# Performance work log

Hardware: AMD Instinct MI355X
Metric: run time of the kernel (lower is better)

Reference implementation:

```python
import jax, jax.numpy as jnp
import numpy as np

N_NODES = 50000
N_EDGES = 1600000
IN_SIZE = 128
NUM_HEADS = 4
OUT_SIZE = 32


def setup_inputs() -> dict:
    key = jax.random.key(0)
    k1, k2, k3, k4 = jax.random.split(key, 4)
    feat = jax.random.normal(k1, (N_NODES, IN_SIZE), dtype=jnp.float32)
    src = jax.random.randint(k2, (N_EDGES,), 0, N_NODES)
    dst = jnp.sort(jax.random.randint(k3, (N_EDGES,), 0, N_NODES))
    # fc weight of DGL DotGatConv: Linear(in_size, num_heads*out_size, bias=False)
    W = jax.random.normal(k4, (IN_SIZE, NUM_HEADS * OUT_SIZE), dtype=jnp.float32) * 0.05
    return {"feat": feat, "src": src, "dst": dst, "W": W}


def reference(feat, src, dst, W):
    N = feat.shape[0]
    H, D = NUM_HEADS, OUT_SIZE
    # project: [N, H, D]
    h = (feat @ W).reshape(N, H, D)
    h_src = h[src]            # [E, H, D] gather
    h_dst = h[dst]            # [E, H, D] gather
    # per-edge dot-product attention score, scaled by sqrt(out_size)
    e = jnp.sum(h_src * h_dst, axis=-1) / jnp.sqrt(jnp.asarray(D, h.dtype))  # [E, H]
    # edge softmax over incoming edges of each destination node
    m = jax.ops.segment_max(e, dst, num_segments=N)        # [N, H]
    ex = jnp.exp(e - m[dst])                               # [E, H]
    s = jax.ops.segment_sum(ex, dst, num_segments=N)       # [N, H]
    alpha = ex / s[dst]                                    # [E, H]
    # weighted aggregation of source features: sum_e alpha_e * h_src_e -> dst
    out = jax.ops.segment_sum(alpha[:, :, None] * h_src, dst, num_segments=N)  # [N, H, D]
    return out
```

## Files before the change

### kernel.cpp

```cpp
#include <hip/hip_runtime.h>
#include <math.h>

#define N_NODES 50000
#define N_EDGES 1600000
#define IN_SIZE 128
#define HD 128
#define NUM_HEADS 4
#define OUT_SIZE 32
#define STRIPS (N_NODES / 16)
#define STRIPS_PER_WAVE 3

#define SCALE2 0.25503486f

typedef __attribute__((ext_vector_type(8))) short short8;
typedef __attribute__((ext_vector_type(4))) float floatx4;

static __device__ __forceinline__ unsigned bf16rne(float f) {
    unsigned u = __float_as_uint(f);
    u += 0x7FFF + ((u >> 16) & 1);
    return u >> 16;
}
static __device__ __forceinline__ float bf16lo(unsigned u) {
    return __uint_as_float(u << 16);
}
static __device__ __forceinline__ float bf16hi(unsigned u) {
    return __uint_as_float(u & 0xFFFF0000u);
}

__global__ __launch_bounds__(256) void k_init(const float* __restrict__ W,
                                              const int* __restrict__ dst,
                                              unsigned short* __restrict__ WT,
                                              int* __restrict__ off) {
    int i = blockIdx.x * 256 + threadIdx.x;
    if (i < IN_SIZE * HD) {
        int c = i >> 7, k = i & 127;
        WT[c * IN_SIZE + k] = (unsigned short)bf16rne(W[k * HD + c]);
    }
    if (i <= N_NODES) {
        int lo = 0, hi = N_EDGES;
        while (lo < hi) {
            int mid = (lo + hi) >> 1;
            if (dst[mid] < i) lo = mid + 1; else hi = mid;
        }
        off[i] = lo;
    }
}

__global__ __launch_bounds__(256, 1) void k_proj(const float* __restrict__ feat,
                                                 const unsigned short* __restrict__ WT,
                                                 unsigned short* __restrict__ hb) {
    int wid = (blockIdx.x * 256 + threadIdx.x) >> 6;
    int lane = threadIdx.x & 63;
    int s0 = wid * STRIPS_PER_WAVE;
    if (s0 >= STRIPS) return;
    int quad = lane >> 4;
    int l15 = lane & 15;

    short8 Bf[8][4];
#pragma unroll
    for (int t = 0; t < 8; t++) {
#pragma unroll
        for (int kb = 0; kb < 4; kb++) {
            union { uint4 v; short8 s; } u;
            u.v = *(const uint4*)(WT + (size_t)(t * 16 + l15) * IN_SIZE + kb * 32 + quad * 8);
            Bf[t][kb] = u.s;
        }
    }

    for (int it = 0; it < STRIPS_PER_WAVE; it++) {
        int strip = s0 + it;
        if (strip >= STRIPS) break;
        int row = strip * 16 + l15;

        const float* ab = feat + (size_t)row * IN_SIZE + quad * 8;
        float4 a[8];
#pragma unroll
        for (int kb = 0; kb < 4; kb++) {
            a[2 * kb]     = *(const float4*)(ab + kb * 32);
            a[2 * kb + 1] = *(const float4*)(ab + kb * 32 + 4);
        }

        floatx4 acc[8];
#pragma unroll
        for (int t = 0; t < 8; t++) acc[t] = (floatx4)(0.f);

#pragma unroll
        for (int kb = 0; kb < 4; kb++) {
            float4 x = a[2 * kb], y = a[2 * kb + 1];
            union { short8 s; unsigned u[4]; } af;
            af.u[0] = bf16rne(x.x) | (bf16rne(x.y) << 16);
            af.u[1] = bf16rne(x.z) | (bf16rne(x.w) << 16);
            af.u[2] = bf16rne(y.x) | (bf16rne(y.y) << 16);
            af.u[3] = bf16rne(y.z) | (bf16rne(y.w) << 16);
#pragma unroll
            for (int t = 0; t < 8; t++)
                acc[t] = __builtin_amdgcn_mfma_f32_16x16x32_bf16(af.s, Bf[t][kb], acc[t], 0, 0, 0);
        }

#pragma unroll
        for (int t = 0; t < 8; t++) {
#pragma unroll
            for (int r = 0; r < 4; r++) {
                int R = strip * 16 + quad * 4 + r;
                hb[(size_t)R * HD + t * 16 + l15] = (unsigned short)bf16rne(acc[t][r]);
            }
        }
    }
}

__global__ __launch_bounds__(256) void k_edge(const unsigned short* __restrict__ hb,
                                              const int* __restrict__ src,
                                              const int* __restrict__ off,
                                              float* __restrict__ out) {
    int n = (blockIdx.x * 256 + threadIdx.x) >> 6;
    int lane = threadIdx.x & 63;
    if (n >= N_NODES) return;
    int e0 = off[n], e1 = off[n + 1];

    int g = lane >> 4;
    int p = lane & 15;

    const uint4* h4 = (const uint4*)hb;
    uint4 hdv = h4[(size_t)n * 16 + p];
    float hd[8];
#pragma unroll
    for (int d = 0; d < 4; d++) {
        unsigned u = ((const unsigned*)&hdv)[d];
        hd[2 * d]     = bf16lo(u) * SCALE2;
        hd[2 * d + 1] = bf16hi(u) * SCALE2;
    }

    float s = 0.f;
    float acc[8];
#pragma unroll
    for (int i = 0; i < 8; i++) acc[i] = 0.f;

    int iters = (e1 - e0 + 3) >> 2;
    int e = e0 + g;
    bool act = (e < e1);
    int si = act ? src[e] : n;
    uint4 a = h4[(size_t)si * 16 + p];

    for (int it = 0; it < iters; it++) {
        int en = e + 4;
        bool act_n = (en < e1);
        int si_n = act_n ? src[en] : n;
        uint4 b = h4[(size_t)si_n * 16 + p];

        float av[8];
#pragma unroll
        for (int d = 0; d < 4; d++) {
            unsigned u = ((const unsigned*)&a)[d];
            av[2 * d]     = bf16lo(u);
            av[2 * d + 1] = bf16hi(u);
        }
        float pd = 0.f;
#pragma unroll
        for (int i = 0; i < 8; i++) pd = fmaf(av[i], hd[i], pd);
        pd += __shfl_xor(pd, 1);
        pd += __shfl_xor(pd, 2);

        float sc = fminf(pd, 30.f);
        float w = act ? __builtin_amdgcn_exp2f(sc) : 0.f;
        s += w;
#pragma unroll
        for (int i = 0; i < 8; i++) acc[i] = fmaf(w, av[i], acc[i]);

        a = b; act = act_n; e = en;
    }

#pragma unroll
    for (int d = 16; d <= 32; d <<= 1) {
        s += __shfl_xor(s, d);
#pragma unroll
        for (int i = 0; i < 8; i++) acc[i] += __shfl_xor(acc[i], d);
    }

    if (g == 0) {
        float inv = (s > 0.f) ? 1.f / s : 0.f;
        float4 o0, o1;
        o0.x = acc[0] * inv; o0.y = acc[1] * inv; o0.z = acc[2] * inv; o0.w = acc[3] * inv;
        o1.x = acc[4] * inv; o1.y = acc[5] * inv; o1.z = acc[6] * inv; o1.w = acc[7] * inv;
        float4* op = (float4*)(out + (size_t)n * HD + 8 * p);
        op[0] = o0;
        op[1] = o1;
    }
}

extern "C" void kernel_launch(void* const* d_in, const int* in_sizes, int n_in,
                              void* d_out, int out_size, void* d_ws, size_t ws_size,
                              hipStream_t stream) {
    const float* feat = (const float*)d_in[0];
    const int*   src  = (const int*)d_in[1];
    const int*   dst  = (const int*)d_in[2];
    const float* W    = (const float*)d_in[3];
    float* out = (float*)d_out;

    char* ws = (char*)d_ws;
    unsigned short* hb = (unsigned short*)ws;
    unsigned short* WT = (unsigned short*)(ws + (size_t)N_NODES * HD * 2);
    int* off = (int*)(ws + (size_t)N_NODES * HD * 2 + IN_SIZE * HD * 2);

    k_init<<<(N_NODES + 1 + 255) / 256, 256, 0, stream>>>(W, dst, WT, off);
    int proj_waves = (STRIPS + STRIPS_PER_WAVE - 1) / STRIPS_PER_WAVE;
    k_proj<<<(proj_waves + 3) / 4, 256, 0, stream>>>(feat, WT, hb);
    k_edge<<<(N_NODES + 3) / 4, 256, 0, stream>>>(hb, src, off, out);
}
```

Measured before the change: 154.7 us.

## Split projected features per head and assign one wave per (head, node)

New measurement: 189.8 us. 1.23x slower.

```diff
diff --git a/kernel.cpp b/kernel.cpp
--- a/kernel.cpp
+++ b/kernel.cpp
@@ -9,6 +9,9 @@
 #define OUT_SIZE 32
 #define STRIPS (N_NODES / 16)
 #define STRIPS_PER_WAVE 3
+#define PROJ_WAVES ((STRIPS + STRIPS_PER_WAVE - 1) / STRIPS_PER_WAVE)
+#define PROJ_BLOCKS ((PROJ_WAVES + 3) / 4)
+#define OFF_BLOCKS ((N_NODES + 1 + 255) / 256)
 
 #define SCALE2 0.25503486f
 
@@ -27,29 +30,25 @@
     return __uint_as_float(u & 0xFFFF0000u);
 }
 
-__global__ __launch_bounds__(256) void k_init(const float* __restrict__ W,
-                                              const int* __restrict__ dst,
-                                              unsigned short* __restrict__ WT,
-                                              int* __restrict__ off) {
-    int i = blockIdx.x * 256 + threadIdx.x;
-    if (i < IN_SIZE * HD) {
-        int c = i >> 7, k = i & 127;
-        WT[c * IN_SIZE + k] = (unsigned short)bf16rne(W[k * HD + c]);
-    }
-    if (i <= N_NODES) {
-        int lo = 0, hi = N_EDGES;
-        while (lo < hi) {
-            int mid = (lo + hi) >> 1;
-            if (dst[mid] < i) lo = mid + 1; else hi = mid;
-        }
-        off[i] = lo;
-    }
-}
-
-__global__ __launch_bounds__(256, 1) void k_proj(const float* __restrict__ feat,
-                                                 const unsigned short* __restrict__ WT,
-                                                 unsigned short* __restrict__ hb) {
-    int wid = (blockIdx.x * 256 + threadIdx.x) >> 6;
+__global__ __launch_bounds__(256, 1) void k_pre(const float* __restrict__ feat,
+                                                const float* __restrict__ W,
+                                                const int* __restrict__ dst,
+                                                unsigned short* __restrict__ hh,
+                                                int* __restrict__ off) {
+    if (blockIdx.x >= PROJ_BLOCKS) {
+        int i = (blockIdx.x - PROJ_BLOCKS) * 256 + threadIdx.x;
+        if (i <= N_NODES) {
+            int lo = 0, hi = N_EDGES;
+            while (lo < hi) {
+                int mid = (lo + hi) >> 1;
+                if (dst[mid] < i) lo = mid + 1; else hi = mid;
+            }
+            off[i] = lo;
+        }
+        return;
+    }
+
+    int wid = blockIdx.x * 4 + (threadIdx.x >> 6);
     int lane = threadIdx.x & 63;
     int s0 = wid * STRIPS_PER_WAVE;
     if (s0 >= STRIPS) return;
@@ -61,9 +60,15 @@
     for (int t = 0; t < 8; t++) {
 #pragma unroll
         for (int kb = 0; kb < 4; kb++) {
-            union { uint4 v; short8 s; } u;
-            u.v = *(const uint4*)(WT + (size_t)(t * 16 + l15) * IN_SIZE + kb * 32 + quad * 8);
-            Bf[t][kb] = u.s;
+            union { short8 s; unsigned u[4]; } bu;
+#pragma unroll
+            for (int jj = 0; jj < 4; jj++) {
+                int k0 = kb * 32 + quad * 8 + 2 * jj;
+                float lo = W[(size_t)k0 * HD + t * 16 + l15];
+                float hi = W[(size_t)(k0 + 1) * HD + t * 16 + l15];
+                bu.u[jj] = bf16rne(lo) | (bf16rne(hi) << 16);
+            }
+            Bf[t][kb] = bu.s;
         }
     }
 
@@ -102,32 +107,37 @@
 #pragma unroll
             for (int r = 0; r < 4; r++) {
                 int R = strip * 16 + quad * 4 + r;
-                hb[(size_t)R * HD + t * 16 + l15] = (unsigned short)bf16rne(acc[t][r]);
+                hh[((size_t)(t >> 1) * N_NODES + R) * 32 + (t & 1) * 16 + l15] =
+                    (unsigned short)bf16rne(acc[t][r]);
             }
         }
     }
 }
 
-__global__ __launch_bounds__(256) void k_edge(const unsigned short* __restrict__ hb,
+__global__ __launch_bounds__(256) void k_edge(const unsigned short* __restrict__ hh,
                                               const int* __restrict__ src,
                                               const int* __restrict__ off,
                                               float* __restrict__ out) {
-    int n = (blockIdx.x * 256 + threadIdx.x) >> 6;
+    int wid = blockIdx.x * 4 + (threadIdx.x >> 6);
     int lane = threadIdx.x & 63;
-    if (n >= N_NODES) return;
+    if (wid >= 4 * N_NODES) return;
+    int hd = (wid >= 3 * N_NODES) ? 3 : (wid >= 2 * N_NODES) ? 2 : (wid >= N_NODES) ? 1 : 0;
+    int n = wid - hd * N_NODES;
+
     int e0 = off[n], e1 = off[n + 1];
-
-    int g = lane >> 4;
-    int p = lane & 15;
-
-    const uint4* h4 = (const uint4*)hb;
-    uint4 hdv = h4[(size_t)n * 16 + p];
-    float hd[8];
+    int g = lane >> 2;
+    int q = lane & 3;
+
+    const uint4* h4 = (const uint4*)hh;
+    size_t hbase = (size_t)hd * N_NODES;
+
+    uint4 hdv = h4[(hbase + n) * 4 + q];
+    float hdc[8];
 #pragma unroll
     for (int d = 0; d < 4; d++) {
         unsigned u = ((const unsigned*)&hdv)[d];
-        hd[2 * d]     = bf16lo(u) * SCALE2;
-        hd[2 * d + 1] = bf16hi(u) * SCALE2;
+        hdc[2 * d]     = bf16lo(u) * SCALE2;
+        hdc[2 * d + 1] = bf16hi(u) * SCALE2;
     }
 
     float s = 0.f;
@@ -135,17 +145,17 @@
 #pragma unroll
     for (int i = 0; i < 8; i++) acc[i] = 0.f;
 
-    int iters = (e1 - e0 + 3) >> 2;
+    int iters = (e1 - e0 + 15) >> 4;
     int e = e0 + g;
     bool act = (e < e1);
     int si = act ? src[e] : n;
-    uint4 a = h4[(size_t)si * 16 + p];
+    uint4 a = h4[(hbase + si) * 4 + q];
 
     for (int it = 0; it < iters; it++) {
-        int en = e + 4;
+        int en = e + 16;
         bool act_n = (en < e1);
         int si_n = act_n ? src[en] : n;
-        uint4 b = h4[(size_t)si_n * 16 + p];
+        uint4 b = h4[(hbase + si_n) * 4 + q];
 
         float av[8];
 #pragma unroll
@@ -156,7 +166,7 @@
         }
         float pd = 0.f;
 #pragma unroll
-        for (int i = 0; i < 8; i++) pd = fmaf(av[i], hd[i], pd);
+        for (int i = 0; i < 8; i++) pd = fmaf(av[i], hdc[i], pd);
         pd += __shfl_xor(pd, 1);
         pd += __shfl_xor(pd, 2);
 
@@ -170,7 +180,7 @@
     }
 
 #pragma unroll
-    for (int d = 16; d <= 32; d <<= 1) {
+    for (int d = 4; d <= 32; d <<= 1) {
         s += __shfl_xor(s, d);
 #pragma unroll
         for (int i = 0; i < 8; i++) acc[i] += __shfl_xor(acc[i], d);
@@ -181,7 +191,7 @@
         float4 o0, o1;
         o0.x = acc[0] * inv; o0.y = acc[1] * inv; o0.z = acc[2] * inv; o0.w = acc[3] * inv;
         o1.x = acc[4] * inv; o1.y = acc[5] * inv; o1.z = acc[6] * inv; o1.w = acc[7] * inv;
-        float4* op = (float4*)(out + (size_t)n * HD + 8 * p);
+        float4* op = (float4*)(out + (size_t)n * HD + hd * 32 + q * 8);
         op[0] = o0;
         op[1] = o1;
     }
@@ -197,12 +207,9 @@
     float* out = (float*)d_out;
 
     char* ws = (char*)d_ws;
-    unsigned short* hb = (unsigned short*)ws;
-    unsigned short* WT = (unsigned short*)(ws + (size_t)N_NODES * HD * 2);
-    int* off = (int*)(ws + (size_t)N_NODES * HD * 2 + IN_SIZE * HD * 2);
-
-    k_init<<<(N_NODES + 1 + 255) / 256, 256, 0, stream>>>(W, dst, WT, off);
-    int proj_waves = (STRIPS + STRIPS_PER_WAVE - 1) / STRIPS_PER_WAVE;
-    k_proj<<<(proj_waves + 3) / 4, 256, 0, stream>>>(feat, WT, hb);
-    k_edge<<<(N_NODES + 3) / 4, 256, 0, stream>>>(hb, src, off, out);
-}
+    unsigned short* hh = (unsigned short*)ws;
+    int* off = (int*)(ws + (size_t)NUM_HEADS * N_NODES * 32 * 2);
+
+    k_pre<<<PROJ_BLOCKS + OFF_BLOCKS, 256, 0, stream>>>(feat, W, dst, hh, off);
+    k_edge<<<(4 * N_NODES + 3) / 4, 256, 0, stream>>>(hh, src, off, out);
+}
```
